# Performance work log

Measured on AMD Instinct MI355X. Metric: run time of the kernel, lower is better.

## Reference

```python
import jax, jax.numpy as jnp
import numpy as np

B, S, D = 2, 2048, 2048
H, HD, RD = 16, 128, 64
ND = HD - RD  # nope head dim = 64
QR, KVR = 1536, 512  # q/kv lora ranks
EPS = 1e-6


def rmsnorm(x, w):
    return x * jax.lax.rsqrt(jnp.mean(x * x, axis=-1, keepdims=True) + EPS) * w


def rope_rotate(x, cos, sin):
    # x: [B, h, S, r]; cos/sin: [S, r/2]; pairwise complex rotation
    xr, xi = x[..., 0::2], x[..., 1::2]
    o_r = xr * cos - xi * sin
    o_i = xr * sin + xi * cos
    return jnp.stack([o_r, o_i], axis=-1).reshape(x.shape)


def setup_inputs() -> dict:
    key = jax.random.key(0)
    ks = jax.random.split(key, 12)
    sd = 0.02
    # rotary tables for rope_head_dim
    inv_freq = 1.0 / (10000.0 ** (np.arange(0, RD, 2, dtype=np.float32) / RD))
    t = np.arange(S, dtype=np.float32)
    ang = np.outer(t, inv_freq)  # [S, RD/2]
    return {
        "x": jax.random.normal(ks[0], (B, S, D), dtype=jnp.float32),
        "freqs_cos": jnp.asarray(np.cos(ang)),
        "freqs_sin": jnp.asarray(np.sin(ang)),
        "w_cq": jax.random.normal(ks[1], (QR, D), dtype=jnp.float32) * sd,
        "w_dq_nope": jax.random.normal(ks[2], (H * ND, QR), dtype=jnp.float32) * sd,
        "w_dq_rope": jax.random.normal(ks[3], (H * RD, QR), dtype=jnp.float32) * sd,
        "w_ckv": jax.random.normal(ks[4], (KVR, D), dtype=jnp.float32) * sd,
        "w_dk_nope": jax.random.normal(ks[5], (H * ND, KVR), dtype=jnp.float32) * sd,
        "w_dv": jax.random.normal(ks[6], (H * HD, KVR), dtype=jnp.float32) * sd,
        "w_krope": jax.random.normal(ks[7], (RD, D), dtype=jnp.float32) * sd,
        "w_proj": jax.random.normal(ks[8], (H * HD, H * HD), dtype=jnp.float32) * sd,
        "q_norm_w": jnp.ones((QR,), dtype=jnp.float32),
        "kv_norm_w": jnp.ones((KVR,), dtype=jnp.float32),
    }


def reference(x, freqs_cos, freqs_sin, w_cq, w_dq_nope, w_dq_rope, w_ckv,
              w_dk_nope, w_dv, w_krope, w_proj, q_norm_w, kv_norm_w):
    b, s, _ = x.shape
    # low-rank q path
    norm_q = rmsnorm(jnp.einsum("bsd,rd->bsr", x, w_cq), q_norm_w)
    q_nope = jnp.einsum("bsr,or->bso", norm_q, w_dq_nope).reshape(b, s, H, ND).transpose(0, 2, 1, 3)
    q_rope = jnp.einsum("bsr,or->bso", norm_q, w_dq_rope).reshape(b, s, H, RD).transpose(0, 2, 1, 3)
    # low-rank kv path
    norm_kv = rmsnorm(jnp.einsum("bsd,rd->bsr", x, w_ckv), kv_norm_w)
    k_nope = jnp.einsum("bsr,or->bso", norm_kv, w_dk_nope).reshape(b, s, H, ND).transpose(0, 2, 1, 3)
    v = jnp.einsum("bsr,or->bso", norm_kv, w_dv).reshape(b, s, H, HD).transpose(0, 2, 1, 3)
    # shared single-head rope key from x directly
    k_rope_raw = jnp.einsum("bsd,rd->bsr", x, w_krope).reshape(b, s, 1, RD).transpose(0, 2, 1, 3)
    # NOTE: source does `k_rope, q_rope = apply_rope(query_rope, key_rope, cis)`,
    # i.e. the rotated query lands in the K slot and the rotated (1-head) key in the Q slot.
    k_rope = rope_rotate(q_rope, freqs_cos, freqs_sin)            # [B,H,S,RD]
    q_rope_out = rope_rotate(k_rope_raw, freqs_cos, freqs_sin)     # [B,1,S,RD]
    q = jnp.concatenate([q_nope, jnp.broadcast_to(q_rope_out, (b, H, s, RD))], axis=-1)
    k = jnp.concatenate([k_nope, k_rope], axis=-1)
    # causal SDPA, scale 1/sqrt(head_dim)
    scores = jnp.einsum("bhqd,bhkd->bhqk", q, k) / jnp.sqrt(jnp.float32(HD))
    mask = jnp.tril(jnp.ones((s, s), dtype=bool))
    scores = jnp.where(mask, scores, jnp.finfo(scores.dtype).min)
    attn = jax.nn.softmax(scores, axis=-1)
    out = jnp.einsum("bhqk,bhkd->bhqd", attn, v)  # [B,H,S,HD]
    out = out.transpose(0, 2, 1, 3).reshape(b, s, H * HD)
    return jnp.einsum("bso,po->bsp", out, w_proj)
```

## Files before the change

### kernel.cpp

```cpp
#include <hip/hip_runtime.h>

typedef __attribute__((ext_vector_type(4))) float f32x4;
typedef __attribute__((ext_vector_type(8))) short short8;
typedef unsigned short ushort_t;

__device__ __forceinline__ float bf2f(ushort_t u) {
  unsigned int i = ((unsigned int)u) << 16;
  return __builtin_bit_cast(float, i);
}
__device__ __forceinline__ ushort_t f2bf(float f) {
  unsigned int x = __builtin_bit_cast(unsigned int, f);
  unsigned int r = (x + 0x7FFFu + ((x >> 16) & 1u)) >> 16;
  return (ushort_t)r;
}

__global__ __launch_bounds__(256)
void cvt_all(const float* __restrict__ x, const float* __restrict__ wcq,
             const float* __restrict__ wdqn, const float* __restrict__ wdqr,
             const float* __restrict__ wckv, const float* __restrict__ wdkn,
             const float* __restrict__ wdv, const float* __restrict__ wkr,
             const float* __restrict__ wpr,
             ushort_t* ox, ushort_t* owcq, ushort_t* owdqn, ushort_t* owdqr,
             ushort_t* owckv, ushort_t* owdkn, ushort_t* owdv, ushort_t* owkr,
             ushort_t* owpr) {
  int bid = blockIdx.x;
  const float* in; ushort_t* out;
  if (bid < 8192)       { in = x;    out = ox;    }
  else if (bid < 11264) { in = wcq;  out = owcq;  bid -= 8192;  }
  else if (bid < 12800) { in = wdqn; out = owdqn; bid -= 11264; }
  else if (bid < 14336) { in = wdqr; out = owdqr; bid -= 12800; }
  else if (bid < 15360) { in = wckv; out = owckv; bid -= 14336; }
  else if (bid < 15872) { in = wdkn; out = owdkn; bid -= 15360; }
  else if (bid < 16896) { in = wdv;  out = owdv;  bid -= 15872; }
  else if (bid < 17024) { in = wkr;  out = owkr;  bid -= 16896; }
  else                  { in = wpr;  out = owpr;  bid -= 17024; }
  const long i = ((long)bid * 256 + threadIdx.x) * 4;
  float4 v = *(const float4*)(in + i);
  ushort4 o;
  o.x = f2bf(v.x); o.y = f2bf(v.y); o.z = f2bf(v.z); o.w = f2bf(v.w);
  *(ushort4*)(out + i) = o;
}

template <int OUT_BF16>
__global__ __launch_bounds__(256)
void gemm_bt(const ushort_t* __restrict__ A, const ushort_t* __restrict__ B,
             void* __restrict__ Cv, int M, int N, int K) {
  __shared__ __align__(16) ushort_t As[128 * 64];
  __shared__ __align__(16) ushort_t Bs[128 * 64];
  const int tid = threadIdx.x;
  const int lane = tid & 63;
  const int wid = tid >> 6;
  const int m0 = blockIdx.y * 128;
  const int n0 = blockIdx.x * 128;
  const int wm = (wid >> 1) * 64;
  const int wn = (wid & 1) * 64;

  f32x4 acc[4][4];
#pragma unroll
  for (int m = 0; m < 4; ++m)
#pragma unroll
    for (int n = 0; n < 4; ++n) acc[m][n] = (f32x4){0.f, 0.f, 0.f, 0.f};

  const int ktiles = K >> 6;
  for (int kt = 0; kt < ktiles; ++kt) {
    const int k0 = kt << 6;
    __syncthreads();
#pragma unroll
    for (int i = 0; i < 4; ++i) {
      const int chunk = (i * 4 + wid) * 1024;
      const int o = chunk + lane * 16;
      const int row = o >> 7;
      const int cb = o & 127;
      const ushort_t* src = A + (long)(m0 + row) * K + (k0 + (cb >> 1));
      __builtin_amdgcn_global_load_lds((const __attribute__((address_space(1))) unsigned int*)src,
                                       (__attribute__((address_space(3))) unsigned int*)((char*)As + chunk),
                                       16, 0, 0);
    }
#pragma unroll
    for (int i = 0; i < 4; ++i) {
      const int chunk = (i * 4 + wid) * 1024;
      const int o = chunk + lane * 16;
      const int row = o >> 7;
      const int cb = o & 127;
      int brow = n0 + row;
      if (brow > N - 1) brow = N - 1;
      const ushort_t* src = B + (long)brow * K + (k0 + (cb >> 1));
      __builtin_amdgcn_global_load_lds((const __attribute__((address_space(1))) unsigned int*)src,
                                       (__attribute__((address_space(3))) unsigned int*)((char*)Bs + chunk),
                                       16, 0, 0);
    }
    __syncthreads();
#pragma unroll
    for (int kk = 0; kk < 2; ++kk) {
      const int kb = kk * 32 + ((lane >> 4) << 3);
      short8 a[4], b[4];
#pragma unroll
      for (int m = 0; m < 4; ++m)
        a[m] = *(const short8*)(As + (wm + m * 16 + (lane & 15)) * 64 + kb);
#pragma unroll
      for (int n = 0; n < 4; ++n)
        b[n] = *(const short8*)(Bs + (wn + n * 16 + (lane & 15)) * 64 + kb);
#pragma unroll
      for (int m = 0; m < 4; ++m)
#pragma unroll
        for (int n = 0; n < 4; ++n)
          acc[m][n] = __builtin_amdgcn_mfma_f32_16x16x32_bf16(a[m], b[n], acc[m][n], 0, 0, 0);
    }
  }
  const int rb = m0 + wm + ((lane >> 4) << 2);
  const int cbase = n0 + wn + (lane & 15);
#pragma unroll
  for (int m = 0; m < 4; ++m)
#pragma unroll
    for (int n = 0; n < 4; ++n) {
      const int c = cbase + n * 16;
      if (c < N) {
#pragma unroll
        for (int j = 0; j < 4; ++j) {
          const long r = rb + m * 16 + j;
          if (OUT_BF16)
            ((ushort_t*)Cv)[r * N + c] = f2bf(acc[m][n][j]);
          else
            ((float*)Cv)[r * N + c] = acc[m][n][j];
        }
      }
    }
}

__global__ __launch_bounds__(256)
void gemm_bt3(const ushort_t* __restrict__ A,
              const ushort_t* __restrict__ B0, ushort_t* __restrict__ C0, int nb0, int N0,
              const ushort_t* __restrict__ B1, ushort_t* __restrict__ C1, int nb1, int N1,
              const ushort_t* __restrict__ B2, ushort_t* __restrict__ C2, int N2,
              int K) {
  __shared__ __align__(16) ushort_t As[128 * 64];
  __shared__ __align__(16) ushort_t Bs[128 * 64];
  int bx = blockIdx.x;
  const ushort_t* Bp; ushort_t* Cp; int N;
  if (bx < nb0)            { Bp = B0; Cp = C0; N = N0; }
  else if (bx < nb0 + nb1) { Bp = B1; Cp = C1; N = N1; bx -= nb0; }
  else                     { Bp = B2; Cp = C2; N = N2; bx -= nb0 + nb1; }
  const int tid = threadIdx.x;
  const int lane = tid & 63;
  const int wid = tid >> 6;
  const int m0 = blockIdx.y * 128;
  const int n0 = bx * 128;
  const int wm = (wid >> 1) * 64;
  const int wn = (wid & 1) * 64;

  f32x4 acc[4][4];
#pragma unroll
  for (int m = 0; m < 4; ++m)
#pragma unroll
    for (int n = 0; n < 4; ++n) acc[m][n] = (f32x4){0.f, 0.f, 0.f, 0.f};

  const int ktiles = K >> 6;
  for (int kt = 0; kt < ktiles; ++kt) {
    const int k0 = kt << 6;
    __syncthreads();
#pragma unroll
    for (int i = 0; i < 4; ++i) {
      const int chunk = (i * 4 + wid) * 1024;
      const int o = chunk + lane * 16;
      const int row = o >> 7;
      const int cb = o & 127;
      const ushort_t* src = A + (long)(m0 + row) * K + (k0 + (cb >> 1));
      __builtin_amdgcn_global_load_lds((const __attribute__((address_space(1))) unsigned int*)src,
                                       (__attribute__((address_space(3))) unsigned int*)((char*)As + chunk),
                                       16, 0, 0);
    }
#pragma unroll
    for (int i = 0; i < 4; ++i) {
      const int chunk = (i * 4 + wid) * 1024;
      const int o = chunk + lane * 16;
      const int row = o >> 7;
      const int cb = o & 127;
      int brow = n0 + row;
      if (brow > N - 1) brow = N - 1;
      const ushort_t* src = Bp + (long)brow * K + (k0 + (cb >> 1));
      __builtin_amdgcn_global_load_lds((const __attribute__((address_space(1))) unsigned int*)src,
                                       (__attribute__((address_space(3))) unsigned int*)((char*)Bs + chunk),
                                       16, 0, 0);
    }
    __syncthreads();
#pragma unroll
    for (int kk = 0; kk < 2; ++kk) {
      const int kb = kk * 32 + ((lane >> 4) << 3);
      short8 a[4], b[4];
#pragma unroll
      for (int m = 0; m < 4; ++m)
        a[m] = *(const short8*)(As + (wm + m * 16 + (lane & 15)) * 64 + kb);
#pragma unroll
      for (int n = 0; n < 4; ++n)
        b[n] = *(const short8*)(Bs + (wn + n * 16 + (lane & 15)) * 64 + kb);
#pragma unroll
      for (int m = 0; m < 4; ++m)
#pragma unroll
        for (int n = 0; n < 4; ++n)
          acc[m][n] = __builtin_amdgcn_mfma_f32_16x16x32_bf16(a[m], b[n], acc[m][n], 0, 0, 0);
    }
  }
  const int rb = m0 + wm + ((lane >> 4) << 2);
  const int cbase = n0 + wn + (lane & 15);
#pragma unroll
  for (int m = 0; m < 4; ++m)
#pragma unroll
    for (int n = 0; n < 4; ++n) {
      const int c = cbase + n * 16;
      if (c < N) {
#pragma unroll
        for (int j = 0; j < 4; ++j) {
          const long r = rb + m * 16 + j;
          Cp[r * N + c] = f2bf(acc[m][n][j]);
        }
      }
    }
}

__device__ __forceinline__ void rms_body(const ushort_t* x, const float* w,
                                         ushort_t* out, int R, float* warr) {
  const int tid = threadIdx.x;
  float ss = 0.f;
  for (int i = tid; i < R; i += 256) { float v = bf2f(x[i]); ss += v * v; }
#pragma unroll
  for (int off = 32; off; off >>= 1) ss += __shfl_xor(ss, off);
  if ((tid & 63) == 0) warr[tid >> 6] = ss;
  __syncthreads();
  const float tot = warr[0] + warr[1] + warr[2] + warr[3];
  const float rs = rsqrtf(tot / (float)R + 1e-6f);
  for (int i = tid; i < R; i += 256) out[i] = f2bf(bf2f(x[i]) * rs * w[i]);
}

__global__ __launch_bounds__(256)
void rmsnorm_both(const ushort_t* __restrict__ ckv, const float* __restrict__ kvnw,
                  ushort_t* __restrict__ nkv,
                  const ushort_t* __restrict__ cq, const float* __restrict__ qnw,
                  ushort_t* __restrict__ nq) {
  __shared__ float warr[4];
  const int bid = blockIdx.x;
  if (bid < 4096) rms_body(ckv + (long)bid * 512, kvnw, nkv + (long)bid * 512, 512, warr);
  else {
    const long row = bid - 4096;
    rms_body(cq + row * 1536, qnw, nq + row * 1536, 1536, warr);
  }
}

__device__ __forceinline__ void rope_body(const ushort_t* in, ushort_t* out,
                                          const float* fc, const float* fs,
                                          int heads, int bid) {
  const int idx = bid * 256 + threadIdx.x;
  const int i = idx & 31;
  const int rest = idx >> 5;
  const int hh = rest % heads;
  const int row = rest / heads;
  const int srow = row & 2047;
  const float c = fc[srow * 32 + i];
  const float s = fs[srow * 32 + i];
  const long base = (long)row * heads * 64 + hh * 64 + 2 * i;
  const float x0 = bf2f(in[base]);
  const float x1 = bf2f(in[base + 1]);
  out[base] = f2bf(x0 * c - x1 * s);
  out[base + 1] = f2bf(x0 * s + x1 * c);
}

__global__ __launch_bounds__(256)
void rope_kraw(const ushort_t* __restrict__ kraw, ushort_t* __restrict__ qrs,
               const float* __restrict__ fc, const float* __restrict__ fs) {
  rope_body(kraw, qrs, fc, fs, 1, blockIdx.x);
}

__global__ __launch_bounds__(256)
void tv_rope(const ushort_t* __restrict__ v, ushort_t* __restrict__ vt,
             const ushort_t* __restrict__ qr, ushort_t* __restrict__ krope,
             const float* __restrict__ fc, const float* __restrict__ fs) {
  __shared__ __align__(16) ushort_t Ts[64 * 128];
  const int bid = blockIdx.x;
  if (bid >= 1024) { rope_body(qr, krope, fc, fs, 16, bid - 1024); return; }
  const int t = threadIdx.x;
  const int bh = bid >> 5;
  const int b = bh >> 4, h = bh & 15;
  const int s0 = (bid & 31) * 64;
#pragma unroll
  for (int i = 0; i < 4; ++i) {
    const int c = t + 256 * i;
    const int si = c >> 4;
    const int xb = (c & 15) * 16;
    const long src = ((long)b * 2048 + s0 + si) * 2048 + h * 128 + (xb >> 1);
    short8 val = *(const short8*)(v + src);
    *(short8*)((char*)Ts + si * 256 + (xb ^ ((si & 15) << 4))) = val;
  }
  __syncthreads();
  const int d = (t & 63) + ((t >> 7) << 6);
  const int scb = ((t >> 6) & 1) * 4;
#pragma unroll
  for (int i = 0; i < 4; ++i) {
    const int sc = scb + i;
    short8 val;
#pragma unroll
    for (int j = 0; j < 8; ++j) {
      const int s = sc * 8 + j;
      val[j] = (short)*(const ushort_t*)((const char*)Ts + s * 256 + ((2 * d) ^ ((s & 15) << 4)));
    }
    *(short8*)(vt + ((long)bh * 128 + d) * 2048 + s0 + sc * 8) = val;
  }
}

__global__ __launch_bounds__(512)
void attn_mfma(const ushort_t* __restrict__ qn, const ushort_t* __restrict__ qrs,
               const ushort_t* __restrict__ kn, const ushort_t* __restrict__ kr,
               const ushort_t* __restrict__ vt, ushort_t* __restrict__ out) {
  __shared__ __align__(16) ushort_t Ks[2][8192];
  __shared__ __align__(16) ushort_t Vts[2][8192];
  __shared__ __align__(16) ushort_t Ps[8192];
  const int tid = threadIdx.x, lane = tid & 63, wid = tid >> 6;
  const int g = lane >> 4, lq = lane & 15;
  const int bh = blockIdx.x, b = bh >> 4, h = bh & 15;
  const float scale = 0.08838834764831845f;
  char* Pbase = (char*)Ps + wid * 2048;

  auto stage = [&](int bsel, int kt) {
    const int k0s = kt * 64;
#pragma unroll
    for (int i = 0; i < 2; ++i) {
      const int cc = wid * 2 + i;
      const int o = cc * 1024 + lane * 16;
      {
        const int row = o >> 8;
        const int dK = ((o & 255) ^ ((row & 7) << 4)) >> 1;
        const long krow = (long)b * 2048 + k0s + row;
        const ushort_t* srcK = (dK < 64) ? (kn + krow * 1024 + h * 64 + dK)
                                         : (kr + krow * 1024 + h * 64 + (dK - 64));
        __builtin_amdgcn_global_load_lds((const __attribute__((address_space(1))) unsigned int*)srcK,
            (__attribute__((address_space(3))) unsigned int*)((char*)Ks[bsel] + cc * 1024), 16, 0, 0);
      }
      {
        const int dr = o >> 7;
        const int se = ((o & 127) ^ ((dr & 7) << 4)) >> 1;
        const ushort_t* srcV = vt + ((long)bh * 128 + dr) * 2048 + k0s + se;
        __builtin_amdgcn_global_load_lds((const __attribute__((address_space(1))) unsigned int*)srcV,
            (__attribute__((address_space(3))) unsigned int*)((char*)Vts[bsel] + cc * 1024), 16, 0, 0);
      }
    }
  };

  const int pair = blockIdx.y;
  for (int half = 0; half < 2; ++half) {
    const int t = half ? (15 - pair) : pair;
    const int q0 = t * 128;
    const int qw0 = q0 + wid * 16;
    short8 aq[4];
    {
      const long grow = (long)b * 2048 + qw0 + lq;
#pragma unroll
      for (int ks = 0; ks < 4; ++ks) {
        const int d = ks * 32 + g * 8;
        const ushort_t* src = (d < 64) ? (qn + grow * 1024 + h * 64 + d)
                                       : (qrs + grow * 64 + (d - 64));
        aq[ks] = *(const short8*)src;
      }
    }
    f32x4 oacc[8];
#pragma unroll
    for (int n = 0; n < 8; ++n) oacc[n] = (f32x4){0.f, 0.f, 0.f, 0.f};
    float sm[4] = {-3e38f, -3e38f, -3e38f, -3e38f};
    float sl[4] = {0.f, 0.f, 0.f, 0.f};

    const int kmax = 2 * t + 2;
    int cur = 0;
    stage(0, 0);
    for (int kt = 0; kt < kmax; ++kt) {
      const int k0 = kt * 64;
      if (kt < kmax - 1) {
        stage(cur ^ 1, kt + 1);
        asm volatile("s_waitcnt vmcnt(4)" ::: "memory");
      } else {
        asm volatile("s_waitcnt vmcnt(0)" ::: "memory");
      }
      __builtin_amdgcn_s_barrier();
      __builtin_amdgcn_sched_barrier(0);

      f32x4 sacc[4];
#pragma unroll
      for (int n = 0; n < 4; ++n) sacc[n] = (f32x4){0.f, 0.f, 0.f, 0.f};
      __builtin_amdgcn_s_setprio(1);
#pragma unroll
      for (int ks = 0; ks < 4; ++ks) {
        const int x = ks * 64 + g * 16;
#pragma unroll
        for (int n = 0; n < 4; ++n) {
          const int kl = n * 16 + lq;
          short8 bk = *(const short8*)((const char*)Ks[cur] + kl * 256 + (x ^ ((kl & 7) << 4)));
          sacc[n] = __builtin_amdgcn_mfma_f32_16x16x32_bf16(aq[ks], bk, sacc[n], 0, 0, 0);
        }
      }
      __builtin_amdgcn_s_setprio(0);
      if (k0 + 63 > qw0) {
#pragma unroll
        for (int n = 0; n < 4; ++n) {
          const int key = k0 + n * 16 + lq;
#pragma unroll
          for (int j = 0; j < 4; ++j) {
            const int qrow = qw0 + g * 4 + j;
            if (key > qrow) sacc[n][j] = -3e38f;
          }
        }
      }
      float tmax[4];
#pragma unroll
      for (int j = 0; j < 4; ++j)
        tmax[j] = fmaxf(fmaxf(sacc[0][j], sacc[1][j]), fmaxf(sacc[2][j], sacc[3][j]));
#pragma unroll
      for (int off = 1; off < 16; off <<= 1)
#pragma unroll
        for (int j = 0; j < 4; ++j) tmax[j] = fmaxf(tmax[j], __shfl_xor(tmax[j], off));
      bool need = false;
#pragma unroll
      for (int j = 0; j < 4; ++j) {
        tmax[j] *= scale;
        need = need || (tmax[j] > sm[j] + 8.f);
      }
      if (__any(need)) {
#pragma unroll
        for (int j = 0; j < 4; ++j) {
          const float mn = fmaxf(sm[j], tmax[j]);
          const float fr = __expf(sm[j] - mn);
          sm[j] = mn;
          sl[j] *= fr;
#pragma unroll
          for (int n = 0; n < 8; ++n) oacc[n][j] *= fr;
        }
      }
      f32x4 p[4];
#pragma unroll
      for (int n = 0; n < 4; ++n)
#pragma unroll
        for (int j = 0; j < 4; ++j)
          p[n][j] = __expf(__builtin_fmaf(sacc[n][j], scale, -sm[j]));
      float psum[4];
#pragma unroll
      for (int j = 0; j < 4; ++j) psum[j] = p[0][j] + p[1][j] + p[2][j] + p[3][j];
#pragma unroll
      for (int off = 1; off < 16; off <<= 1)
#pragma unroll
        for (int j = 0; j < 4; ++j) psum[j] += __shfl_xor(psum[j], off);
#pragma unroll
      for (int j = 0; j < 4; ++j) sl[j] += psum[j];
#pragma unroll
      for (int n = 0; n < 4; ++n) {
        const int col2 = (n * 16 + lq) * 2;
#pragma unroll
        for (int j = 0; j < 4; ++j) {
          const int row = g * 4 + j;
          *(ushort_t*)(Pbase + row * 128 + (col2 ^ ((row & 7) << 4))) = f2bf(p[n][j]);
        }
      }
      __builtin_amdgcn_s_setprio(1);
#pragma unroll
      for (int ks2 = 0; ks2 < 2; ++ks2) {
        const int x = ks2 * 64 + g * 16;
        short8 pa = *(const short8*)(Pbase + lq * 128 + (x ^ ((lq & 7) << 4)));
#pragma unroll
        for (int nd = 0; nd < 8; ++nd) {
          const int dl = nd * 16 + lq;
          short8 vb = *(const short8*)((const char*)Vts[cur] + dl * 128 + (x ^ ((dl & 7) << 4)));
          oacc[nd] = __builtin_amdgcn_mfma_f32_16x16x32_bf16(pa, vb, oacc[nd], 0, 0, 0);
        }
      }
      __builtin_amdgcn_s_setprio(0);
      __builtin_amdgcn_sched_barrier(0);
      __builtin_amdgcn_s_barrier();
      cur ^= 1;
    }
    float inv[4];
#pragma unroll
    for (int j = 0; j < 4; ++j) inv[j] = 1.f / sl[j];
#pragma unroll
    for (int nd = 0; nd < 8; ++nd) {
      const int d = nd * 16 + lq;
#pragma unroll
      for (int j = 0; j < 4; ++j) {
        const long row = (long)b * 2048 + qw0 + g * 4 + j;
        out[row * 2048 + h * 128 + d] = f2bf(oacc[nd][j] * inv[j]);
      }
    }
  }
}

extern "C" void kernel_launch(void* const* d_in, const int* in_sizes, int n_in,
                              void* d_out, int out_size, void* d_ws, size_t ws_size,
                              hipStream_t stream) {
  const float* x      = (const float*)d_in[0];
  const float* fcos   = (const float*)d_in[1];
  const float* fsin   = (const float*)d_in[2];
  const float* w_cq   = (const float*)d_in[3];
  const float* w_dqn  = (const float*)d_in[4];
  const float* w_dqr  = (const float*)d_in[5];
  const float* w_ckv  = (const float*)d_in[6];
  const float* w_dkn  = (const float*)d_in[7];
  const float* w_dv   = (const float*)d_in[8];
  const float* w_kr   = (const float*)d_in[9];
  const float* w_proj = (const float*)d_in[10];
  const float* qnw    = (const float*)d_in[11];
  const float* kvnw   = (const float*)d_in[12];
  float* out = (float*)d_out;

  char* ws = (char*)d_ws;
  ushort_t* x_bf     = (ushort_t*)(ws + 0);
  ushort_t* wcq_bf   = (ushort_t*)(ws + 16777216);
  ushort_t* wdqn_bf  = (ushort_t*)(ws + 23068672);
  ushort_t* wdqr_bf  = (ushort_t*)(ws + 26214400);
  ushort_t* wckv_bf  = (ushort_t*)(ws + 29360128);
  ushort_t* wdkn_bf  = (ushort_t*)(ws + 31457280);
  ushort_t* wdv_bf   = (ushort_t*)(ws + 32505856);
  ushort_t* wpr_bf   = (ushort_t*)(ws + 34603008);
  ushort_t* cq_bf    = (ushort_t*)(ws + 42991616);
  ushort_t* krope_bf = (ushort_t*)(ws + 42991616);
  ushort_t* qrs_bf   = (ushort_t*)(ws + 51904512);
  ushort_t* ckv_bf   = (ushort_t*)(ws + 55574528);
  ushort_t* nq_bf    = (ushort_t*)(ws + 59768832);
  ushort_t* attn_bf  = (ushort_t*)(ws + 55574528);
  ushort_t* nkv_bf   = (ushort_t*)(ws + 72351744);
  ushort_t* qnope_bf = (ushort_t*)(ws + 76546048);
  ushort_t* kraw_bf  = (ushort_t*)(ws + 76546048);
  ushort_t* qr_bf    = (ushort_t*)(ws + 0);
  ushort_t* knope_bf = (ushort_t*)(ws + 8388608);
  ushort_t* v_bf     = (ushort_t*)(ws + 84934656);
  ushort_t* wkr_bf   = (ushort_t*)(ws + 84934656);
  ushort_t* vt_bf    = (ushort_t*)(ws + 16777216);

  cvt_all<<<21120, 256, 0, stream>>>(x, w_cq, w_dqn, w_dqr, w_ckv, w_dkn, w_dv, w_kr, w_proj,
                                     x_bf, wcq_bf, wdqn_bf, wdqr_bf, wckv_bf, wdkn_bf,
                                     wdv_bf, wkr_bf, wpr_bf);
  gemm_bt3<<<dim3(17, 32), 256, 0, stream>>>(x_bf,
                                             wckv_bf, ckv_bf, 4, 512,
                                             wcq_bf, cq_bf, 12, 1536,
                                             wkr_bf, kraw_bf, 64, 2048);
  rmsnorm_both<<<8192, 256, 0, stream>>>(ckv_bf, kvnw, nkv_bf, cq_bf, qnw, nq_bf);
  rope_kraw<<<512, 256, 0, stream>>>(kraw_bf, qrs_bf, fcos, fsin);
  gemm_bt3<<<dim3(16, 32), 256, 0, stream>>>(nq_bf,
                                             wdqn_bf, qnope_bf, 8, 1024,
                                             wdqr_bf, qr_bf, 8, 1024,
                                             wdqn_bf, qnope_bf, 1024, 1536);
  gemm_bt3<<<dim3(24, 32), 256, 0, stream>>>(nkv_bf,
                                             wdkn_bf, knope_bf, 8, 1024,
                                             wdv_bf, v_bf, 16, 2048,
                                             wdkn_bf, knope_bf, 1024, 512);
  tv_rope<<<9216, 256, 0, stream>>>(v_bf, vt_bf, qr_bf, krope_bf, fcos, fsin);
  attn_mfma<<<dim3(32, 8), 512, 0, stream>>>(qnope_bf, qrs_bf, knope_bf, krope_bf, vt_bf, attn_bf);
  gemm_bt<0><<<dim3(16, 32), 256, 0, stream>>>(attn_bf, wpr_bf, out, 4096, 2048, 2048);
}
```

Before: 345.1 us.

## Give each attention wave two query sub-tiles and one q-tile per block

The attention kernel now runs 4 waves of 256 threads, with each wave handling 32 query rows (two 16-row MFMA tiles) instead of 16. Each K and V fragment read from LDS therefore feeds two MFMAs. The paired-tile loop inside a block is replaced by a 16-wide grid dimension that issues heavy tiles first, so each block processes one 128-row q tile. This halves LDS reads per MFMA and removes the serial two-half loop, at the cost of higher register pressure from doubled accumulators and 4 staging loads per thread.

```diff
diff --git a/kernel.cpp b/kernel.cpp
--- a/kernel.cpp
+++ b/kernel.cpp
@@ -305,13 +305,13 @@
   }
 }
 
-__global__ __launch_bounds__(512)
+__global__ __launch_bounds__(256)
 void attn_mfma(const ushort_t* __restrict__ qn, const ushort_t* __restrict__ qrs,
                const ushort_t* __restrict__ kn, const ushort_t* __restrict__ kr,
                const ushort_t* __restrict__ vt, ushort_t* __restrict__ out) {
   __shared__ __align__(16) ushort_t Ks[2][8192];
   __shared__ __align__(16) ushort_t Vts[2][8192];
-  __shared__ __align__(16) ushort_t Ps[8192];
+  __shared__ __align__(16) ushort_t Ps[4096];
   const int tid = threadIdx.x, lane = tid & 63, wid = tid >> 6;
   const int g = lane >> 4, lq = lane & 15;
   const int bh = blockIdx.x, b = bh >> 4, h = bh & 15;
@@ -321,8 +321,8 @@
   auto stage = [&](int bsel, int kt) {
     const int k0s = kt * 64;
 #pragma unroll
-    for (int i = 0; i < 2; ++i) {
-      const int cc = wid * 2 + i;
+    for (int i = 0; i < 4; ++i) {
+      const int cc = wid * 4 + i;
       const int o = cc * 1024 + lane * 16;
       {
         const int row = o >> 8;
@@ -343,72 +343,88 @@
     }
   };
 
-  const int pair = blockIdx.y;
-  for (int half = 0; half < 2; ++half) {
-    const int t = half ? (15 - pair) : pair;
-    const int q0 = t * 128;
-    const int qw0 = q0 + wid * 16;
-    short8 aq[4];
-    {
-      const long grow = (long)b * 2048 + qw0 + lq;
-#pragma unroll
-      for (int ks = 0; ks < 4; ++ks) {
-        const int d = ks * 32 + g * 8;
-        const ushort_t* src = (d < 64) ? (qn + grow * 1024 + h * 64 + d)
-                                       : (qrs + grow * 64 + (d - 64));
-        aq[ks] = *(const short8*)src;
-      }
-    }
-    f32x4 oacc[8];
-#pragma unroll
-    for (int n = 0; n < 8; ++n) oacc[n] = (f32x4){0.f, 0.f, 0.f, 0.f};
-    float sm[4] = {-3e38f, -3e38f, -3e38f, -3e38f};
-    float sl[4] = {0.f, 0.f, 0.f, 0.f};
-
-    const int kmax = 2 * t + 2;
-    int cur = 0;
-    stage(0, 0);
-    for (int kt = 0; kt < kmax; ++kt) {
-      const int k0 = kt * 64;
-      if (kt < kmax - 1) {
-        stage(cur ^ 1, kt + 1);
-        asm volatile("s_waitcnt vmcnt(4)" ::: "memory");
-      } else {
-        asm volatile("s_waitcnt vmcnt(0)" ::: "memory");
-      }
-      __builtin_amdgcn_s_barrier();
-      __builtin_amdgcn_sched_barrier(0);
-
-      f32x4 sacc[4];
-#pragma unroll
-      for (int n = 0; n < 4; ++n) sacc[n] = (f32x4){0.f, 0.f, 0.f, 0.f};
-      __builtin_amdgcn_s_setprio(1);
-#pragma unroll
-      for (int ks = 0; ks < 4; ++ks) {
-        const int x = ks * 64 + g * 16;
-#pragma unroll
-        for (int n = 0; n < 4; ++n) {
-          const int kl = n * 16 + lq;
-          short8 bk = *(const short8*)((const char*)Ks[cur] + kl * 256 + (x ^ ((kl & 7) << 4)));
-          sacc[n] = __builtin_amdgcn_mfma_f32_16x16x32_bf16(aq[ks], bk, sacc[n], 0, 0, 0);
-        }
-      }
-      __builtin_amdgcn_s_setprio(0);
-      if (k0 + 63 > qw0) {
+  const int y = blockIdx.y;
+  const int t = (y < 8) ? (15 - y) : (y - 8);
+  const int q0 = t * 128;
+  const int qw0 = q0 + wid * 32;
+
+  short8 aq[2][4];
+#pragma unroll
+  for (int m = 0; m < 2; ++m) {
+    const long grow = (long)b * 2048 + qw0 + m * 16 + lq;
+#pragma unroll
+    for (int ks = 0; ks < 4; ++ks) {
+      const int d = ks * 32 + g * 8;
+      const ushort_t* src = (d < 64) ? (qn + grow * 1024 + h * 64 + d)
+                                     : (qrs + grow * 64 + (d - 64));
+      aq[m][ks] = *(const short8*)src;
+    }
+  }
+  f32x4 oacc[2][8];
+#pragma unroll
+  for (int m = 0; m < 2; ++m)
+#pragma unroll
+    for (int n = 0; n < 8; ++n) oacc[m][n] = (f32x4){0.f, 0.f, 0.f, 0.f};
+  float sm[2][4], sl[2][4];
+#pragma unroll
+  for (int m = 0; m < 2; ++m)
+#pragma unroll
+    for (int j = 0; j < 4; ++j) { sm[m][j] = -3e38f; sl[m][j] = 0.f; }
+  short8 pa[2][2];
+
+  const int kmax = 2 * t + 2;
+  int cur = 0;
+  stage(0, 0);
+  for (int kt = 0; kt < kmax; ++kt) {
+    const int k0 = kt * 64;
+    if (kt < kmax - 1) {
+      stage(cur ^ 1, kt + 1);
+      asm volatile("s_waitcnt vmcnt(8)" ::: "memory");
+    } else {
+      asm volatile("s_waitcnt vmcnt(0)" ::: "memory");
+    }
+    __builtin_amdgcn_s_barrier();
+    __builtin_amdgcn_sched_barrier(0);
+
+    f32x4 sacc[2][4];
+#pragma unroll
+    for (int m = 0; m < 2; ++m)
+#pragma unroll
+      for (int n = 0; n < 4; ++n) sacc[m][n] = (f32x4){0.f, 0.f, 0.f, 0.f};
+    __builtin_amdgcn_s_setprio(1);
+#pragma unroll
+    for (int ks = 0; ks < 4; ++ks) {
+      const int x = ks * 64 + g * 16;
+#pragma unroll
+      for (int n = 0; n < 4; ++n) {
+        const int kl = n * 16 + lq;
+        short8 bk = *(const short8*)((const char*)Ks[cur] + kl * 256 + (x ^ ((kl & 7) << 4)));
+        sacc[0][n] = __builtin_amdgcn_mfma_f32_16x16x32_bf16(aq[0][ks], bk, sacc[0][n], 0, 0, 0);
+        sacc[1][n] = __builtin_amdgcn_mfma_f32_16x16x32_bf16(aq[1][ks], bk, sacc[1][n], 0, 0, 0);
+      }
+    }
+    __builtin_amdgcn_s_setprio(0);
+#pragma unroll
+    for (int m = 0; m < 2; ++m) {
+      if (k0 + 63 > qw0 + m * 16) {
 #pragma unroll
         for (int n = 0; n < 4; ++n) {
           const int key = k0 + n * 16 + lq;
 #pragma unroll
           for (int j = 0; j < 4; ++j) {
-            const int qrow = qw0 + g * 4 + j;
-            if (key > qrow) sacc[n][j] = -3e38f;
+            const int qrow = qw0 + m * 16 + g * 4 + j;
+            if (key > qrow) sacc[m][n][j] = -3e38f;
           }
         }
       }
+    }
+#pragma unroll
+    for (int m = 0; m < 2; ++m) {
       float tmax[4];
 #pragma unroll
       for (int j = 0; j < 4; ++j)
-        tmax[j] = fmaxf(fmaxf(sacc[0][j], sacc[1][j]), fmaxf(sacc[2][j], sacc[3][j]));
+        tmax[j] = fmaxf(fmaxf(sacc[m][0][j], sacc[m][1][j]),
+                        fmaxf(sacc[m][2][j], sacc[m][3][j]));
 #pragma unroll
       for (int off = 1; off < 16; off <<= 1)
 #pragma unroll
@@ -417,17 +433,17 @@
 #pragma unroll
       for (int j = 0; j < 4; ++j) {
         tmax[j] *= scale;
-        need = need || (tmax[j] > sm[j] + 8.f);
+        need = need || (tmax[j] > sm[m][j] + 8.f);
       }
       if (__any(need)) {
 #pragma unroll
         for (int j = 0; j < 4; ++j) {
-          const float mn = fmaxf(sm[j], tmax[j]);
-          const float fr = __expf(sm[j] - mn);
-          sm[j] = mn;
-          sl[j] *= fr;
-#pragma unroll
-          for (int n = 0; n < 8; ++n) oacc[n][j] *= fr;
+          const float mn = fmaxf(sm[m][j], tmax[j]);
+          const float fr = __expf(sm[m][j] - mn);
+          sm[m][j] = mn;
+          sl[m][j] *= fr;
+#pragma unroll
+          for (int n = 0; n < 8; ++n) oacc[m][n][j] *= fr;
         }
       }
       f32x4 p[4];
@@ -435,7 +451,7 @@
       for (int n = 0; n < 4; ++n)
 #pragma unroll
         for (int j = 0; j < 4; ++j)
-          p[n][j] = __expf(__builtin_fmaf(sacc[n][j], scale, -sm[j]));
+          p[n][j] = __expf(__builtin_fmaf(sacc[m][n][j], scale, -sm[m][j]));
       float psum[4];
 #pragma unroll
       for (int j = 0; j < 4; ++j) psum[j] = p[0][j] + p[1][j] + p[2][j] + p[3][j];
@@ -444,7 +460,7 @@
 #pragma unroll
         for (int j = 0; j < 4; ++j) psum[j] += __shfl_xor(psum[j], off);
 #pragma unroll
-      for (int j = 0; j < 4; ++j) sl[j] += psum[j];
+      for (int j = 0; j < 4; ++j) sl[m][j] += psum[j];
 #pragma unroll
       for (int n = 0; n < 4; ++n) {
         const int col2 = (n * 16 + lq) * 2;
@@ -454,33 +470,41 @@
           *(ushort_t*)(Pbase + row * 128 + (col2 ^ ((row & 7) << 4))) = f2bf(p[n][j]);
         }
       }
-      __builtin_amdgcn_s_setprio(1);
 #pragma unroll
       for (int ks2 = 0; ks2 < 2; ++ks2) {
         const int x = ks2 * 64 + g * 16;
-        short8 pa = *(const short8*)(Pbase + lq * 128 + (x ^ ((lq & 7) << 4)));
-#pragma unroll
-        for (int nd = 0; nd < 8; ++nd) {
-          const int dl = nd * 16 + lq;
-          short8 vb = *(const short8*)((const char*)Vts[cur] + dl * 128 + (x ^ ((dl & 7) << 4)));
-          oacc[nd] = __builtin_amdgcn_mfma_f32_16x16x32_bf16(pa, vb, oacc[nd], 0, 0, 0);
-        }
-      }
-      __builtin_amdgcn_s_setprio(0);
-      __builtin_amdgcn_sched_barrier(0);
-      __builtin_amdgcn_s_barrier();
-      cur ^= 1;
-    }
+        pa[m][ks2] = *(const short8*)(Pbase + lq * 128 + (x ^ ((lq & 7) << 4)));
+      }
+    }
+    __builtin_amdgcn_s_setprio(1);
+#pragma unroll
+    for (int nd = 0; nd < 8; ++nd) {
+      const int dl = nd * 16 + lq;
+      const int sw = (dl & 7) << 4;
+      short8 vb0 = *(const short8*)((const char*)Vts[cur] + dl * 128 + ((g * 16) ^ sw));
+      short8 vb1 = *(const short8*)((const char*)Vts[cur] + dl * 128 + ((64 + g * 16) ^ sw));
+      oacc[0][nd] = __builtin_amdgcn_mfma_f32_16x16x32_bf16(pa[0][0], vb0, oacc[0][nd], 0, 0, 0);
+      oacc[0][nd] = __builtin_amdgcn_mfma_f32_16x16x32_bf16(pa[0][1], vb1, oacc[0][nd], 0, 0, 0);
+      oacc[1][nd] = __builtin_amdgcn_mfma_f32_16x16x32_bf16(pa[1][0], vb0, oacc[1][nd], 0, 0, 0);
+      oacc[1][nd] = __builtin_amdgcn_mfma_f32_16x16x32_bf16(pa[1][1], vb1, oacc[1][nd], 0, 0, 0);
+    }
+    __builtin_amdgcn_s_setprio(0);
+    __builtin_amdgcn_sched_barrier(0);
+    __builtin_amdgcn_s_barrier();
+    cur ^= 1;
+  }
+#pragma unroll
+  for (int m = 0; m < 2; ++m) {
     float inv[4];
 #pragma unroll
-    for (int j = 0; j < 4; ++j) inv[j] = 1.f / sl[j];
+    for (int j = 0; j < 4; ++j) inv[j] = 1.f / sl[m][j];
 #pragma unroll
     for (int nd = 0; nd < 8; ++nd) {
       const int d = nd * 16 + lq;
 #pragma unroll
       for (int j = 0; j < 4; ++j) {
-        const long row = (long)b * 2048 + qw0 + g * 4 + j;
-        out[row * 2048 + h * 128 + d] = f2bf(oacc[nd][j] * inv[j]);
+        const long row = (long)b * 2048 + qw0 + m * 16 + g * 4 + j;
+        out[row * 2048 + h * 128 + d] = f2bf(oacc[m][nd][j] * inv[j]);
       }
     }
   }
@@ -546,6 +570,6 @@
                                              wdv_bf, v_bf, 16, 2048,
                                              wdkn_bf, knope_bf, 1024, 512);
   tv_rope<<<9216, 256, 0, stream>>>(v_bf, vt_bf, qr_bf, krope_bf, fcos, fsin);
-  attn_mfma<<<dim3(32, 8), 512, 0, stream>>>(qnope_bf, qrs_bf, knope_bf, krope_bf, vt_bf, attn_bf);
+  attn_mfma<<<dim3(32, 16), 256, 0, stream>>>(qnope_bf, qrs_bf, knope_bf, krope_bf, vt_bf, attn_bf);
   gemm_bt<0><<<dim3(16, 32), 256, 0, stream>>>(attn_bf, wpr_bf, out, 4096, 2048, 2048);
 }
```

After: 398.4 us. 15.4% more time.

## Software-pipeline QK^T of next tile with softmax/PV of current tile

Applied to the files above, without the earlier changes.

Splits the K and V staging into separate async loads and restructures the attention loop into a two-tile unrolled software pipeline. The QK^T MFMAs for the next key tile are issued before the softmax and PV of the current tile, so matrix and vector work can overlap. K loads run one tile further ahead than V loads. The cost is a second score accumulator set (more registers) and a doubled P shared buffer. The waits become full vmcnt(0) drains at each barrier, which may expose load latency.

```diff
diff --git a/kernel.cpp b/kernel.cpp
--- a/kernel.cpp
+++ b/kernel.cpp
@@ -311,42 +311,46 @@
                const ushort_t* __restrict__ vt, ushort_t* __restrict__ out) {
   __shared__ __align__(16) ushort_t Ks[2][8192];
   __shared__ __align__(16) ushort_t Vts[2][8192];
-  __shared__ __align__(16) ushort_t Ps[8192];
+  __shared__ __align__(16) ushort_t Ps[16384];
   const int tid = threadIdx.x, lane = tid & 63, wid = tid >> 6;
   const int g = lane >> 4, lq = lane & 15;
   const int bh = blockIdx.x, b = bh >> 4, h = bh & 15;
   const float scale = 0.08838834764831845f;
   char* Pbase = (char*)Ps + wid * 2048;
 
-  auto stage = [&](int bsel, int kt) {
+  auto stageK = [&](int bsel, int kt) {
     const int k0s = kt * 64;
 #pragma unroll
     for (int i = 0; i < 2; ++i) {
       const int cc = wid * 2 + i;
       const int o = cc * 1024 + lane * 16;
-      {
-        const int row = o >> 8;
-        const int dK = ((o & 255) ^ ((row & 7) << 4)) >> 1;
-        const long krow = (long)b * 2048 + k0s + row;
-        const ushort_t* srcK = (dK < 64) ? (kn + krow * 1024 + h * 64 + dK)
-                                         : (kr + krow * 1024 + h * 64 + (dK - 64));
-        __builtin_amdgcn_global_load_lds((const __attribute__((address_space(1))) unsigned int*)srcK,
-            (__attribute__((address_space(3))) unsigned int*)((char*)Ks[bsel] + cc * 1024), 16, 0, 0);
-      }
-      {
-        const int dr = o >> 7;
-        const int se = ((o & 127) ^ ((dr & 7) << 4)) >> 1;
-        const ushort_t* srcV = vt + ((long)bh * 128 + dr) * 2048 + k0s + se;
-        __builtin_amdgcn_global_load_lds((const __attribute__((address_space(1))) unsigned int*)srcV,
-            (__attribute__((address_space(3))) unsigned int*)((char*)Vts[bsel] + cc * 1024), 16, 0, 0);
-      }
+      const int row = o >> 8;
+      const int dK = ((o & 255) ^ ((row & 7) << 4)) >> 1;
+      const long krow = (long)b * 2048 + k0s + row;
+      const ushort_t* srcK = (dK < 64) ? (kn + krow * 1024 + h * 64 + dK)
+                                       : (kr + krow * 1024 + h * 64 + (dK - 64));
+      __builtin_amdgcn_global_load_lds((const __attribute__((address_space(1))) unsigned int*)srcK,
+          (__attribute__((address_space(3))) unsigned int*)((char*)Ks[bsel] + cc * 1024), 16, 0, 0);
+    }
+  };
+  auto stageV = [&](int bsel, int kt) {
+    const int k0s = kt * 64;
+#pragma unroll
+    for (int i = 0; i < 2; ++i) {
+      const int cc = wid * 2 + i;
+      const int o = cc * 1024 + lane * 16;
+      const int dr = o >> 7;
+      const int se = ((o & 127) ^ ((dr & 7) << 4)) >> 1;
+      const ushort_t* srcV = vt + ((long)bh * 128 + dr) * 2048 + k0s + se;
+      __builtin_amdgcn_global_load_lds((const __attribute__((address_space(1))) unsigned int*)srcV,
+          (__attribute__((address_space(3))) unsigned int*)((char*)Vts[bsel] + cc * 1024), 16, 0, 0);
     }
   };
 
   const int pair = blockIdx.y;
   for (int half = 0; half < 2; ++half) {
-    const int t = half ? (15 - pair) : pair;
-    const int q0 = t * 128;
+    const int tq = half ? (15 - pair) : pair;
+    const int q0 = tq * 128;
     const int qw0 = q0 + wid * 16;
     short8 aq[4];
     {
@@ -365,23 +369,10 @@
     float sm[4] = {-3e38f, -3e38f, -3e38f, -3e38f};
     float sl[4] = {0.f, 0.f, 0.f, 0.f};
 
-    const int kmax = 2 * t + 2;
-    int cur = 0;
-    stage(0, 0);
-    for (int kt = 0; kt < kmax; ++kt) {
-      const int k0 = kt * 64;
-      if (kt < kmax - 1) {
-        stage(cur ^ 1, kt + 1);
-        asm volatile("s_waitcnt vmcnt(4)" ::: "memory");
-      } else {
-        asm volatile("s_waitcnt vmcnt(0)" ::: "memory");
-      }
-      __builtin_amdgcn_s_barrier();
-      __builtin_amdgcn_sched_barrier(0);
-
-      f32x4 sacc[4];
+    auto qk = [&](f32x4 (&sacc)[4], int u) {
 #pragma unroll
       for (int n = 0; n < 4; ++n) sacc[n] = (f32x4){0.f, 0.f, 0.f, 0.f};
+      const ushort_t* Kbuf = Ks[u & 1];
       __builtin_amdgcn_s_setprio(1);
 #pragma unroll
       for (int ks = 0; ks < 4; ++ks) {
@@ -389,11 +380,14 @@
 #pragma unroll
         for (int n = 0; n < 4; ++n) {
           const int kl = n * 16 + lq;
-          short8 bk = *(const short8*)((const char*)Ks[cur] + kl * 256 + (x ^ ((kl & 7) << 4)));
+          short8 bk = *(const short8*)((const char*)Kbuf + kl * 256 + (x ^ ((kl & 7) << 4)));
           sacc[n] = __builtin_amdgcn_mfma_f32_16x16x32_bf16(aq[ks], bk, sacc[n], 0, 0, 0);
         }
       }
       __builtin_amdgcn_s_setprio(0);
+    };
+    auto process = [&](f32x4 (&sacc)[4], int u) {
+      const int k0 = u * 64;
       if (k0 + 63 > qw0) {
 #pragma unroll
         for (int n = 0; n < 4; ++n) {
@@ -454,6 +448,7 @@
           *(ushort_t*)(Pbase + row * 128 + (col2 ^ ((row & 7) << 4))) = f2bf(p[n][j]);
         }
       }
+      const ushort_t* Vbuf = Vts[u & 1];
       __builtin_amdgcn_s_setprio(1);
 #pragma unroll
       for (int ks2 = 0; ks2 < 2; ++ks2) {
@@ -462,14 +457,35 @@
 #pragma unroll
         for (int nd = 0; nd < 8; ++nd) {
           const int dl = nd * 16 + lq;
-          short8 vb = *(const short8*)((const char*)Vts[cur] + dl * 128 + (x ^ ((dl & 7) << 4)));
+          short8 vb = *(const short8*)((const char*)Vbuf + dl * 128 + (x ^ ((dl & 7) << 4)));
           oacc[nd] = __builtin_amdgcn_mfma_f32_16x16x32_bf16(pa, vb, oacc[nd], 0, 0, 0);
         }
       }
       __builtin_amdgcn_s_setprio(0);
+    };
+
+    const int kmax = 2 * tq + 2;
+    f32x4 saccA[4], saccB[4];
+    stageK(0, 0); stageV(0, 0); stageK(1, 1);
+    asm volatile("s_waitcnt vmcnt(0)" ::: "memory");
+    __builtin_amdgcn_s_barrier();
+    __builtin_amdgcn_sched_barrier(0);
+    qk(saccA, 0);
+    for (int u = 0; u < kmax; u += 2) {
+      if (u + 2 < kmax) stageK(0, u + 2);
+      stageV(1, u + 1);
+      qk(saccB, u + 1);
+      process(saccA, u);
+      asm volatile("s_waitcnt vmcnt(0)" ::: "memory");
+      __builtin_amdgcn_s_barrier();
       __builtin_amdgcn_sched_barrier(0);
+      if (u + 3 < kmax) stageK(1, u + 3);
+      if (u + 2 < kmax) stageV(0, u + 2);
+      if (u + 2 < kmax) qk(saccA, u + 2);
+      process(saccB, u + 1);
+      asm volatile("s_waitcnt vmcnt(0)" ::: "memory");
       __builtin_amdgcn_s_barrier();
-      cur ^= 1;
+      __builtin_amdgcn_sched_barrier(0);
     }
     float inv[4];
 #pragma unroll
```

Result: no change. 341.0 us (-1.2%).
